# Performance work log

Measured on AMD Instinct MI355X. Metric: run time of the kernel, lower is better.

Reference implementation:

```python
import jax, jax.numpy as jnp
import numpy as np

N = 50000  # num nodes


def _spmm(edge_index, edge_w, x):
    # sparse [N,N] @ dense [N,d] via gather + segment-sum
    row, col = edge_index[0], edge_index[1]
    msgs = edge_w[:, None] * x[col]                      # [E, d]
    return jax.ops.segment_sum(msgs, row, num_segments=N)


def setup_inputs() -> dict:
    key = jax.random.key(0)
    k1, k2, k3, k4, k5 = jax.random.split(key, 5)
    E1, E2, d = 800000, 1600000, 128
    x = jax.random.normal(k1, (N, d), dtype=jnp.float32)
    edge_index1 = jax.random.randint(k2, (2, E1), 0, N, dtype=jnp.int64)
    edge_w1 = jax.random.uniform(k3, (E1,), dtype=jnp.float32)
    edge_index2 = jax.random.randint(k4, (2, E2), 0, N, dtype=jnp.int64)
    edge_w2 = jax.random.uniform(k5, (E2,), dtype=jnp.float32)
    return {"x": x, "edge_index1": edge_index1, "edge_w1": edge_w1,
            "edge_index2": edge_index2, "edge_w2": edge_w2}


def reference(x, edge_index1, edge_w1, edge_index2, edge_w2):
    x1 = _spmm(edge_index1, edge_w1, x)   # adj_t  @ x  -> [N, d]
    x2 = _spmm(edge_index2, edge_w2, x)   # adj_t2 @ x  -> [N, d]
    return jnp.concatenate([x1, x2], axis=1)  # [N, 2d]
```

## Files before the change

### kernel.cpp

```cpp
#include <hip/hip_runtime.h>


#define N_NODES 50000
#define D 128
#define OUT_STRIDE 256

#define BSHIFT 6
#define BROWS 64
#define NBUCK ((N_NODES + BROWS - 1) >> BSHIFT)
#define BBITS 10
#define CHUNK 8192
#define WSEG (CHUNK / 8)
#define SITERS (WSEG / 64)
#define CAPB 3072

typedef float vf2 __attribute__((ext_vector_type(2)));

static inline size_t align256(size_t x) { return (x + 255) & ~(size_t)255; }

__device__ __forceinline__ unsigned f32_to_bf16_bits(float f) {
    unsigned u = __float_as_uint(f);
    return (u + 0x7fffu + ((u >> 16) & 1u)) >> 16;
}

template<int BITS>
__device__ __forceinline__ unsigned long long wave_match(int v, bool valid) {
    unsigned long long m = __ballot(valid ? 1 : 0);
    #pragma unroll
    for (int k = 0; k < BITS; ++k) {
        unsigned long long vb = __ballot((v >> k) & 1);
        m &= ((v >> k) & 1) ? vb : ~vb;
    }
    return m;
}


__global__ void __launch_bounds__(512, 4) prep(
        const int* __restrict__ ei1, const float* __restrict__ w1, int E1, int nch1,
        const int* __restrict__ ei2, const float* __restrict__ w2, int E2, int ncht,
        uint2* __restrict__ inter, int* __restrict__ ends,
        const float* __restrict__ x, uint2* __restrict__ xb4, int n4) {
    int bid = blockIdx.x;
    if (bid >= ncht) {
        int i = (bid - ncht) * 512 + threadIdx.x;
        if (i < n4) {
            float4 v = ((const float4*)x)[i];
            unsigned a = f32_to_bf16_bits(v.x);
            unsigned b = f32_to_bf16_bits(v.y);
            unsigned c = f32_to_bf16_bits(v.z);
            unsigned d = f32_to_bf16_bits(v.w);
            xb4[i] = make_uint2(a | (b << 16), c | (d << 16));
        }
        return;
    }
    int cid = bid;
    int g = (cid < nch1) ? 0 : 1;
    int chunk = g ? cid - nch1 : cid;
    const int*   ei = g ? ei2 : ei1;
    const float* w  = g ? w2  : w1;
    int E           = g ? E2  : E1;
    int e0  = chunk * CHUNK;
    int cnt = min(CHUNK, E - e0);

    __shared__ uint2 stage[CHUNK];
    __shared__ unsigned short hwc[8][NBUCK];
    __shared__ int wsum[8];
    int t = threadIdx.x, lane = t & 63, wid = t >> 6;
    unsigned long long below = (1ull << lane) - 1ull;
    for (int i = t; i < (8 * NBUCK) / 2; i += 512) ((int*)hwc)[i] = 0;
    __syncthreads();

    int s0 = wid * WSEG, s1 = min(cnt, s0 + WSEG);
    unsigned meta[SITERS];
    unsigned recs[SITERS];
    #pragma unroll
    for (int k = 0; k < SITERS; ++k) {
        int i = s0 + k * 64 + lane;
        bool v = (i < s1);
        int row = v ? ei[e0 + i] : 0;
        int col = v ? ei[E + e0 + i] : 0;
        float wv = v ? w[e0 + i] : 0.f;
        int bb = row >> BSHIFT;
        unsigned long long m = wave_match<BBITS>(bb, v);
        unsigned rank = (unsigned)__popcll(m & below);
        unsigned base = hwc[wid][bb];
        if (v && (m & below) == 0)
            hwc[wid][bb] = (unsigned short)(base + (unsigned)__popcll(m));
        meta[k] = (unsigned)bb | ((unsigned)(row & 63) << 10) | ((base + rank) << 16);
        recs[k] = (unsigned)col | (f32_to_bf16_bits(wv) << 16);
    }
    __syncthreads();
    {
        int b0 = 2 * t, b1 = b0 + 1;
        int h0[8], h1[8];
        int t0 = 0, t1 = 0;
        if (b0 < NBUCK) {
            #pragma unroll
            for (int q = 0; q < 8; ++q) { h0[q] = hwc[q][b0]; t0 += h0[q]; }
        }
        if (b1 < NBUCK) {
            #pragma unroll
            for (int q = 0; q < 8; ++q) { h1[q] = hwc[q][b1]; t1 += h1[q]; }
        }
        int p = t0 + t1, s = p;
        #pragma unroll
        for (int d2 = 1; d2 < 64; d2 <<= 1) { int u = __shfl_up(s, d2, 64); if (lane >= d2) s += u; }
        if (lane == 63) wsum[wid] = s;
        __syncthreads();
        int add = 0;
        #pragma unroll
        for (int k = 0; k < 8; ++k) if (k < wid) add += wsum[k];
        s += add;
        int excl = s - p;
        if (b0 < NBUCK) {
            int a = excl;
            #pragma unroll
            for (int q = 0; q < 8; ++q) { int h = h0[q]; hwc[q][b0] = (unsigned short)a; a += h; }
            ends[(size_t)cid * NBUCK + b0] = a;
        }
        if (b1 < NBUCK) {
            int a = excl + t0;
            #pragma unroll
            for (int q = 0; q < 8; ++q) { int h = h1[q]; hwc[q][b1] = (unsigned short)a; a += h; }
            ends[(size_t)cid * NBUCK + b1] = a;
        }
    }
    __syncthreads();
    #pragma unroll
    for (int k = 0; k < SITERS; ++k) {
        int i = s0 + k * 64 + lane;
        if (i < s1) {
            unsigned mk = meta[k];
            unsigned bb = mk & 1023u;
            unsigned rlv = (mk >> 10) & 63u;
            unsigned pos = mk >> 16;
            unsigned base = hwc[wid][bb];
            stage[base + pos] = make_uint2(rlv, recs[k]);
        }
    }
    __syncthreads();
    for (int i = t; i < cnt; i += 512)
        inter[(size_t)cid * CHUNK + i] = stage[i];
}


__device__ __forceinline__ void fma_rec(unsigned p, unsigned rec, float& ax, float& ay) {
    float w = __int_as_float((int)(rec & 0xffff0000u));
    ax += w * __int_as_float((int)(p << 16));
    ay += w * __int_as_float((int)(p & 0xffff0000u));
}

__global__ void __launch_bounds__(512, 4) bucket_accum(
        const uint2* __restrict__ inter, const int* __restrict__ ends,
        const unsigned* __restrict__ xb,
        float* __restrict__ out, int nch1, int nch2) {
    int b = blockIdx.x, g = blockIdx.y;
    int c0 = g ? nch1 : 0;
    int nc = g ? nch2 : nch1;

    __shared__ unsigned char rl[CAPB];
    __shared__ unsigned recs[CAPB];
    __shared__ unsigned outb[CAPB];
    __shared__ int crow[BROWS], cur[BROWS], rstart[BROWS];
    __shared__ int total;
    int t = threadIdx.x, lane = t & 63, wid = t >> 6;
    if (t < BROWS) crow[t] = 0;
    if (t == 0) total = 0;
    __syncthreads();
    for (int ci = t; ci < nc; ci += 512) {
        const int* ep = ends + (size_t)(c0 + ci) * NBUCK;
        int s = b ? ep[b - 1] : 0;
        int e = ep[b];
        int n = e - s;
        if (!n) continue;
        int dst = atomicAdd(&total, n);
        const uint2* src = inter + (size_t)(c0 + ci) * CHUNK + s;
        int k = 0;
        for (; k + 2 <= n; k += 2) {
            uint2 a  = src[k];
            uint2 b2 = src[k + 1];
            int p0 = dst + k, p1 = dst + k + 1;
            if (p0 < CAPB) { rl[p0] = (unsigned char)a.x;  recs[p0] = a.y;  atomicAdd(&crow[a.x], 1); }
            if (p1 < CAPB) { rl[p1] = (unsigned char)b2.x; recs[p1] = b2.y; atomicAdd(&crow[b2.x], 1); }
        }
        if (k < n) {
            uint2 a = src[k];
            int p0 = dst + k;
            if (p0 < CAPB) { rl[p0] = (unsigned char)a.x; recs[p0] = a.y; atomicAdd(&crow[a.x], 1); }
        }
    }
    __syncthreads();
    int cnt = min(total, CAPB);
    if (wid == 0) {
        int v = crow[lane], s = v;
        #pragma unroll
        for (int d = 1; d < 64; d <<= 1) { int u = __shfl_up(s, d, 64); if (lane >= d) s += u; }
        cur[lane] = s - v;
        rstart[lane] = s - v;
    }
    __syncthreads();
    for (int i = t; i < cnt; i += 512) {
        int pos = atomicAdd(&cur[rl[i]], 1);
        outb[pos] = recs[i];
    }
    __syncthreads();
    for (int r = wid * 8; r < wid * 8 + 8; ++r) {
        int grow = (b << BSHIFT) + r;
        if (grow >= N_NODES) break;
        int s0 = rstart[r], e0 = cur[r];
        float ax = 0.f, ay = 0.f;
        int j = s0;
        for (; j + 4 <= e0; j += 4) {
            unsigned c0r = outb[j];
            unsigned c1 = outb[j + 1];
            unsigned c2 = outb[j + 2];
            unsigned c3 = outb[j + 3];
            unsigned p0 = xb[(size_t)(c0r & 0xffffu) * 64 + lane];
            unsigned p1 = xb[(size_t)(c1 & 0xffffu) * 64 + lane];
            unsigned p2 = xb[(size_t)(c2 & 0xffffu) * 64 + lane];
            unsigned p3 = xb[(size_t)(c3 & 0xffffu) * 64 + lane];
            fma_rec(p0, c0r, ax, ay);
            fma_rec(p1, c1, ax, ay);
            fma_rec(p2, c2, ax, ay);
            fma_rec(p3, c3, ax, ay);
        }
        for (; j < e0; ++j) {
            unsigned c = outb[j];
            unsigned p = xb[(size_t)(c & 0xffffu) * 64 + lane];
            fma_rec(p, c, ax, ay);
        }
        vf2 rv; rv.x = ax; rv.y = ay;
        vf2* o = (vf2*)(out + (size_t)grow * OUT_STRIDE + g * D);
        __builtin_nontemporal_store(rv, o + lane);
    }
}


__global__ void spmm_scatter(const float* __restrict__ x,
                             const int* __restrict__ ei,
                             const float* __restrict__ w,
                             float* __restrict__ out,
                             int E, int col_off) {
    long long gid = (long long)blockIdx.x * blockDim.x + threadIdx.x;
    int e    = (int)(gid >> 5);
    int lane = (int)(gid & 31);
    if (e >= E) return;
    int row  = ei[e];
    int col  = ei[E + e];
    float wv = w[e];
    const float4* xv = (const float4*)(x + (size_t)col * D);
    float4 v = xv[lane];
    float* o = out + (size_t)row * OUT_STRIDE + col_off + lane * 4;
    atomicAdd(o + 0, wv * v.x);
    atomicAdd(o + 1, wv * v.y);
    atomicAdd(o + 2, wv * v.z);
    atomicAdd(o + 3, wv * v.w);
}

extern "C" void kernel_launch(void* const* d_in, const int* in_sizes, int n_in,
                              void* d_out, int out_size, void* d_ws, size_t ws_size,
                              hipStream_t stream) {
    const float* x   = (const float*)d_in[0];
    const int*   ei1 = (const int*)d_in[1];
    const float* w1  = (const float*)d_in[2];
    const int*   ei2 = (const int*)d_in[3];
    const float* w2  = (const float*)d_in[4];
    float* out = (float*)d_out;

    const int E1 = in_sizes[1] / 2;
    const int E2 = in_sizes[3] / 2;
    const int block = 256;

    int nch1 = (E1 + CHUNK - 1) / CHUNK;
    int nch2 = (E2 + CHUNK - 1) / CHUNK;
    int ncht = nch1 + nch2;

    size_t ends_b  = align256((size_t)ncht * NBUCK * sizeof(int));
    size_t inter_b = align256((size_t)ncht * CHUNK * sizeof(uint2));
    size_t xb_b    = align256((size_t)N_NODES * 64 * sizeof(unsigned));
    size_t o_ends  = 0;
    size_t o_int   = o_ends + ends_b;
    size_t o_xb    = o_int + inter_b;
    size_t needed  = o_xb + xb_b;

    bool ok = (nch1 <= 512) && (nch2 <= 512);

    if (ws_size < needed || !ok) {
        (void)hipMemsetAsync(d_out, 0, (size_t)out_size * sizeof(float), stream);
        long long th1 = (long long)E1 * 32;
        spmm_scatter<<<(int)((th1 + block - 1) / block), block, 0, stream>>>(
            x, ei1, w1, out, E1, 0);
        long long th2 = (long long)E2 * 32;
        spmm_scatter<<<(int)((th2 + block - 1) / block), block, 0, stream>>>(
            x, ei2, w2, out, E2, D);
        return;
    }

    char* ws = (char*)d_ws;
    int*      ends  = (int*)(ws + o_ends);
    uint2*    inter = (uint2*)(ws + o_int);
    unsigned* xb    = (unsigned*)(ws + o_xb);

    {
        int n4 = N_NODES * 32;
        int ncvt = (n4 + 511) / 512;
        prep<<<ncht + ncvt, 512, 0, stream>>>(
            ei1, w1, E1, nch1, ei2, w2, E2, ncht,
            inter, ends, x, (uint2*)xb, n4);
    }

    {
        dim3 gr(NBUCK, 2);
        bucket_accum<<<gr, 512, 0, stream>>>(inter, ends, xb, out, nch1, nch2);
    }
}
```

Before: 212.9 us.

## Fuse prep and bucket accumulation into one cooperative kernel with grid sync

```diff
diff --git a/kernel.cpp b/kernel.cpp
--- a/kernel.cpp
+++ b/kernel.cpp
@@ -1,4 +1,5 @@
 #include <hip/hip_runtime.h>
+#include <hip/hip_cooperative_groups.h>
 
 
 #define N_NODES 50000
@@ -9,10 +10,26 @@
 #define BROWS 64
 #define NBUCK ((N_NODES + BROWS - 1) >> BSHIFT)
 #define BBITS 10
-#define CHUNK 8192
-#define WSEG (CHUNK / 8)
+#define CHUNK 5120
+#define NTHR 1024
+#define NWAVE 16
+#define WSEG (CHUNK / NWAVE)
 #define SITERS (WSEG / 64)
-#define CAPB 3072
+#define ACAP 4096
+#define GRID 512
+
+#define SM_SIZE 50688
+#define SO_REC  0
+#define SO_RL   20480
+#define SO_HWC  25600
+#define SO_WSUM 50624
+#define AO_RECS 0
+#define AO_OUTB 16384
+#define AO_RL   32768
+#define AO_CROW 36864
+#define AO_CUR  37120
+#define AO_RST  37376
+#define AO_TOT  37632
 
 typedef float vf2 __attribute__((ext_vector_type(2)));
 
@@ -35,25 +52,30 @@
 }
 
 
-__global__ void __launch_bounds__(512, 4) prep(
+__device__ __forceinline__ void dev_cvt(const float* __restrict__ x,
+                                        unsigned* __restrict__ xb, int n4) {
+    for (long long i = (long long)blockIdx.x * NTHR + threadIdx.x; i < n4;
+         i += (long long)gridDim.x * NTHR) {
+        float4 v = ((const float4*)x)[i];
+        unsigned a = f32_to_bf16_bits(v.x);
+        unsigned b = f32_to_bf16_bits(v.y);
+        unsigned c = f32_to_bf16_bits(v.z);
+        unsigned d = f32_to_bf16_bits(v.w);
+        ((uint2*)xb)[i] = make_uint2(a | (b << 16), c | (d << 16));
+    }
+}
+
+
+__device__ void dev_scatter(int cid,
         const int* __restrict__ ei1, const float* __restrict__ w1, int E1, int nch1,
-        const int* __restrict__ ei2, const float* __restrict__ w2, int E2, int ncht,
-        uint2* __restrict__ inter, int* __restrict__ ends,
-        const float* __restrict__ x, uint2* __restrict__ xb4, int n4) {
-    int bid = blockIdx.x;
-    if (bid >= ncht) {
-        int i = (bid - ncht) * 512 + threadIdx.x;
-        if (i < n4) {
-            float4 v = ((const float4*)x)[i];
-            unsigned a = f32_to_bf16_bits(v.x);
-            unsigned b = f32_to_bf16_bits(v.y);
-            unsigned c = f32_to_bf16_bits(v.z);
-            unsigned d = f32_to_bf16_bits(v.w);
-            xb4[i] = make_uint2(a | (b << 16), c | (d << 16));
-        }
-        return;
-    }
-    int cid = bid;
+        const int* __restrict__ ei2, const float* __restrict__ w2, int E2,
+        unsigned* __restrict__ irec, unsigned char* __restrict__ irl,
+        int* __restrict__ ends, char* sm) {
+    unsigned*       stage_rec = (unsigned*)(sm + SO_REC);
+    unsigned char*  stage_rl  = (unsigned char*)(sm + SO_RL);
+    unsigned short* hwc       = (unsigned short*)(sm + SO_HWC);
+    int*            wsum      = (int*)(sm + SO_WSUM);
+
     int g = (cid < nch1) ? 0 : 1;
     int chunk = g ? cid - nch1 : cid;
     const int*   ei = g ? ei2 : ei1;
@@ -62,12 +84,9 @@
     int e0  = chunk * CHUNK;
     int cnt = min(CHUNK, E - e0);
 
-    __shared__ uint2 stage[CHUNK];
-    __shared__ unsigned short hwc[8][NBUCK];
-    __shared__ int wsum[8];
     int t = threadIdx.x, lane = t & 63, wid = t >> 6;
     unsigned long long below = (1ull << lane) - 1ull;
-    for (int i = t; i < (8 * NBUCK) / 2; i += 512) ((int*)hwc)[i] = 0;
+    for (int i = t; i < (NWAVE * NBUCK) / 2; i += NTHR) ((int*)hwc)[i] = 0;
     __syncthreads();
 
     int s0 = wid * WSEG, s1 = min(cnt, s0 + WSEG);
@@ -83,46 +102,37 @@
         int bb = row >> BSHIFT;
         unsigned long long m = wave_match<BBITS>(bb, v);
         unsigned rank = (unsigned)__popcll(m & below);
-        unsigned base = hwc[wid][bb];
+        unsigned base = hwc[wid * NBUCK + bb];
         if (v && (m & below) == 0)
-            hwc[wid][bb] = (unsigned short)(base + (unsigned)__popcll(m));
+            hwc[wid * NBUCK + bb] = (unsigned short)(base + (unsigned)__popcll(m));
         meta[k] = (unsigned)bb | ((unsigned)(row & 63) << 10) | ((base + rank) << 16);
         recs[k] = (unsigned)col | (f32_to_bf16_bits(wv) << 16);
     }
     __syncthreads();
     {
-        int b0 = 2 * t, b1 = b0 + 1;
-        int h0[8], h1[8];
-        int t0 = 0, t1 = 0;
-        if (b0 < NBUCK) {
+        int tot = 0;
+        if (t < NBUCK) {
             #pragma unroll
-            for (int q = 0; q < 8; ++q) { h0[q] = hwc[q][b0]; t0 += h0[q]; }
-        }
-        if (b1 < NBUCK) {
-            #pragma unroll
-            for (int q = 0; q < 8; ++q) { h1[q] = hwc[q][b1]; t1 += h1[q]; }
-        }
-        int p = t0 + t1, s = p;
+            for (int q = 0; q < NWAVE; ++q) tot += hwc[q * NBUCK + t];
+        }
+        int s = tot;
         #pragma unroll
         for (int d2 = 1; d2 < 64; d2 <<= 1) { int u = __shfl_up(s, d2, 64); if (lane >= d2) s += u; }
         if (lane == 63) wsum[wid] = s;
         __syncthreads();
         int add = 0;
         #pragma unroll
-        for (int k = 0; k < 8; ++k) if (k < wid) add += wsum[k];
+        for (int k = 0; k < NWAVE; ++k) if (k < wid) add += wsum[k];
         s += add;
-        int excl = s - p;
-        if (b0 < NBUCK) {
-            int a = excl;
+        if (t < NBUCK) {
+            int a = s - tot;
             #pragma unroll
-            for (int q = 0; q < 8; ++q) { int h = h0[q]; hwc[q][b0] = (unsigned short)a; a += h; }
-            ends[(size_t)cid * NBUCK + b0] = a;
-        }
-        if (b1 < NBUCK) {
-            int a = excl + t0;
-            #pragma unroll
-            for (int q = 0; q < 8; ++q) { int h = h1[q]; hwc[q][b1] = (unsigned short)a; a += h; }
-            ends[(size_t)cid * NBUCK + b1] = a;
+            for (int q = 0; q < NWAVE; ++q) {
+                int hq = hwc[q * NBUCK + t];
+                hwc[q * NBUCK + t] = (unsigned short)a;
+                a += hq;
+            }
+            ends[(size_t)cid * NBUCK + t] = a;
         }
     }
     __syncthreads();
@@ -132,15 +142,16 @@
         if (i < s1) {
             unsigned mk = meta[k];
             unsigned bb = mk & 1023u;
-            unsigned rlv = (mk >> 10) & 63u;
-            unsigned pos = mk >> 16;
-            unsigned base = hwc[wid][bb];
-            stage[base + pos] = make_uint2(rlv, recs[k]);
-        }
-    }
-    __syncthreads();
-    for (int i = t; i < cnt; i += 512)
-        inter[(size_t)cid * CHUNK + i] = stage[i];
+            unsigned pos = (mk >> 16) + hwc[wid * NBUCK + bb];
+            stage_rec[pos] = recs[k];
+            stage_rl[pos] = (unsigned char)((mk >> 10) & 63u);
+        }
+    }
+    __syncthreads();
+    for (int i = t; i < cnt; i += NTHR) {
+        irec[(size_t)cid * CHUNK + i] = stage_rec[i];
+        irl[(size_t)cid * CHUNK + i]  = stage_rl[i];
+    }
 }
 
 
@@ -150,89 +161,133 @@
     ay += w * __int_as_float((int)(p & 0xffff0000u));
 }
 
-__global__ void __launch_bounds__(512, 4) bucket_accum(
-        const uint2* __restrict__ inter, const int* __restrict__ ends,
-        const unsigned* __restrict__ xb,
-        float* __restrict__ out, int nch1, int nch2) {
-    int b = blockIdx.x, g = blockIdx.y;
+__device__ void dev_accum(int b, int g, int nch1, int nch2,
+        const unsigned* __restrict__ irec, const unsigned char* __restrict__ irl,
+        const int* __restrict__ ends, const unsigned* __restrict__ xb,
+        float* __restrict__ out, char* sm) {
+    unsigned*      arecs = (unsigned*)(sm + AO_RECS);
+    unsigned*      aoutb = (unsigned*)(sm + AO_OUTB);
+    unsigned char* arl   = (unsigned char*)(sm + AO_RL);
+    int* crow   = (int*)(sm + AO_CROW);
+    int* cur    = (int*)(sm + AO_CUR);
+    int* rstart = (int*)(sm + AO_RST);
+    int* total  = (int*)(sm + AO_TOT);
+
     int c0 = g ? nch1 : 0;
     int nc = g ? nch2 : nch1;
-
-    __shared__ unsigned char rl[CAPB];
-    __shared__ unsigned recs[CAPB];
-    __shared__ unsigned outb[CAPB];
-    __shared__ int crow[BROWS], cur[BROWS], rstart[BROWS];
-    __shared__ int total;
     int t = threadIdx.x, lane = t & 63, wid = t >> 6;
     if (t < BROWS) crow[t] = 0;
-    if (t == 0) total = 0;
-    __syncthreads();
-    for (int ci = t; ci < nc; ci += 512) {
+    if (t == 0) *total = 0;
+    __syncthreads();
+    for (int ci = t; ci < nc; ci += NTHR) {
         const int* ep = ends + (size_t)(c0 + ci) * NBUCK;
         int s = b ? ep[b - 1] : 0;
         int e = ep[b];
         int n = e - s;
         if (!n) continue;
-        int dst = atomicAdd(&total, n);
-        const uint2* src = inter + (size_t)(c0 + ci) * CHUNK + s;
+        int dst = atomicAdd(total, n);
+        const unsigned* sr = irec + (size_t)(c0 + ci) * CHUNK + s;
+        const unsigned char* sl = irl + (size_t)(c0 + ci) * CHUNK + s;
         int k = 0;
         for (; k + 2 <= n; k += 2) {
-            uint2 a  = src[k];
-            uint2 b2 = src[k + 1];
+            unsigned r0 = sr[k], r1 = sr[k + 1];
+            unsigned char l0 = sl[k], l1 = sl[k + 1];
             int p0 = dst + k, p1 = dst + k + 1;
-            if (p0 < CAPB) { rl[p0] = (unsigned char)a.x;  recs[p0] = a.y;  atomicAdd(&crow[a.x], 1); }
-            if (p1 < CAPB) { rl[p1] = (unsigned char)b2.x; recs[p1] = b2.y; atomicAdd(&crow[b2.x], 1); }
+            if (p0 < ACAP) { arl[p0] = l0; arecs[p0] = r0; atomicAdd(&crow[l0], 1); }
+            if (p1 < ACAP) { arl[p1] = l1; arecs[p1] = r1; atomicAdd(&crow[l1], 1); }
         }
         if (k < n) {
-            uint2 a = src[k];
+            unsigned r0 = sr[k];
+            unsigned char l0 = sl[k];
             int p0 = dst + k;
-            if (p0 < CAPB) { rl[p0] = (unsigned char)a.x; recs[p0] = a.y; atomicAdd(&crow[a.x], 1); }
-        }
-    }
-    __syncthreads();
-    int cnt = min(total, CAPB);
+            if (p0 < ACAP) { arl[p0] = l0; arecs[p0] = r0; atomicAdd(&crow[l0], 1); }
+        }
+    }
+    __syncthreads();
+    int cnt = min(*total, ACAP);
     if (wid == 0) {
         int v = crow[lane], s = v;
         #pragma unroll
-        for (int d = 1; d < 64; d <<= 1) { int u = __shfl_up(s, d, 64); if (lane >= d) s += u; }
+        for (int d2 = 1; d2 < 64; d2 <<= 1) { int u = __shfl_up(s, d2, 64); if (lane >= d2) s += u; }
         cur[lane] = s - v;
         rstart[lane] = s - v;
     }
     __syncthreads();
-    for (int i = t; i < cnt; i += 512) {
-        int pos = atomicAdd(&cur[rl[i]], 1);
-        outb[pos] = recs[i];
-    }
-    __syncthreads();
-    for (int r = wid * 8; r < wid * 8 + 8; ++r) {
+    for (int i = t; i < cnt; i += NTHR) {
+        int pos = atomicAdd(&cur[arl[i]], 1);
+        aoutb[pos] = arecs[i];
+    }
+    __syncthreads();
+    for (int r = wid * 4; r < wid * 4 + 4; ++r) {
         int grow = (b << BSHIFT) + r;
         if (grow >= N_NODES) break;
-        int s0 = rstart[r], e0 = cur[r];
+        int rs = rstart[r], re = cur[r];
         float ax = 0.f, ay = 0.f;
-        int j = s0;
-        for (; j + 4 <= e0; j += 4) {
-            unsigned c0r = outb[j];
-            unsigned c1 = outb[j + 1];
-            unsigned c2 = outb[j + 2];
-            unsigned c3 = outb[j + 3];
+        int j = rs;
+        for (; j + 4 <= re; j += 4) {
+            unsigned c0r = aoutb[j];
+            unsigned c1r = aoutb[j + 1];
+            unsigned c2r = aoutb[j + 2];
+            unsigned c3r = aoutb[j + 3];
             unsigned p0 = xb[(size_t)(c0r & 0xffffu) * 64 + lane];
-            unsigned p1 = xb[(size_t)(c1 & 0xffffu) * 64 + lane];
-            unsigned p2 = xb[(size_t)(c2 & 0xffffu) * 64 + lane];
-            unsigned p3 = xb[(size_t)(c3 & 0xffffu) * 64 + lane];
+            unsigned p1 = xb[(size_t)(c1r & 0xffffu) * 64 + lane];
+            unsigned p2 = xb[(size_t)(c2r & 0xffffu) * 64 + lane];
+            unsigned p3 = xb[(size_t)(c3r & 0xffffu) * 64 + lane];
             fma_rec(p0, c0r, ax, ay);
-            fma_rec(p1, c1, ax, ay);
-            fma_rec(p2, c2, ax, ay);
-            fma_rec(p3, c3, ax, ay);
-        }
-        for (; j < e0; ++j) {
-            unsigned c = outb[j];
-            unsigned p = xb[(size_t)(c & 0xffffu) * 64 + lane];
-            fma_rec(p, c, ax, ay);
+            fma_rec(p1, c1r, ax, ay);
+            fma_rec(p2, c2r, ax, ay);
+            fma_rec(p3, c3r, ax, ay);
+        }
+        for (; j < re; ++j) {
+            unsigned cr = aoutb[j];
+            unsigned p = xb[(size_t)(cr & 0xffffu) * 64 + lane];
+            fma_rec(p, cr, ax, ay);
         }
         vf2 rv; rv.x = ax; rv.y = ay;
         vf2* o = (vf2*)(out + (size_t)grow * OUT_STRIDE + g * D);
         __builtin_nontemporal_store(rv, o + lane);
     }
+}
+
+
+__global__ void __launch_bounds__(NTHR, 8) k_fused(
+        const int* ei1, const float* w1, int E1, int nch1,
+        const int* ei2, const float* w2, int E2, int nch2, int ncht,
+        unsigned* irec, unsigned char* irl, int* ends,
+        const float* x, unsigned* xb, int n4, float* out) {
+    __shared__ alignas(16) char sm[SM_SIZE];
+    dev_cvt(x, xb, n4);
+    if ((int)blockIdx.x < ncht)
+        dev_scatter(blockIdx.x, ei1, w1, E1, nch1, ei2, w2, E2, irec, irl, ends, sm);
+    cooperative_groups::this_grid().sync();
+    for (int task = blockIdx.x; task < 2 * NBUCK; task += gridDim.x) {
+        int g = task >= NBUCK;
+        int b = g ? task - NBUCK : task;
+        __syncthreads();
+        dev_accum(b, g, nch1, nch2, irec, irl, ends, xb, out, sm);
+    }
+}
+
+
+__global__ void __launch_bounds__(NTHR, 8) k_prep(
+        const int* ei1, const float* w1, int E1, int nch1,
+        const int* ei2, const float* w2, int E2, int ncht,
+        unsigned* irec, unsigned char* irl, int* ends,
+        const float* x, unsigned* xb, int n4) {
+    __shared__ alignas(16) char sm[SM_SIZE];
+    dev_cvt(x, xb, n4);
+    if ((int)blockIdx.x < ncht)
+        dev_scatter(blockIdx.x, ei1, w1, E1, nch1, ei2, w2, E2, irec, irl, ends, sm);
+}
+
+__global__ void __launch_bounds__(NTHR, 8) k_accum(
+        const unsigned* irec, const unsigned char* irl, const int* ends,
+        const unsigned* xb, float* out, int nch1, int nch2) {
+    __shared__ alignas(16) char sm[AO_TOT + 16];
+    int task = blockIdx.x;
+    int g = task >= NBUCK;
+    int b = g ? task - NBUCK : task;
+    dev_accum(b, g, nch1, nch2, irec, irl, ends, xb, out, sm);
 }
 
 
@@ -260,57 +315,64 @@
 extern "C" void kernel_launch(void* const* d_in, const int* in_sizes, int n_in,
                               void* d_out, int out_size, void* d_ws, size_t ws_size,
                               hipStream_t stream) {
-    const float* x   = (const float*)d_in[0];
-    const int*   ei1 = (const int*)d_in[1];
-    const float* w1  = (const float*)d_in[2];
-    const int*   ei2 = (const int*)d_in[3];
-    const float* w2  = (const float*)d_in[4];
-    float* out = (float*)d_out;
-
-    const int E1 = in_sizes[1] / 2;
-    const int E2 = in_sizes[3] / 2;
+    const int*   ei1_p = (const int*)d_in[1];
+    const float* w1_p  = (const float*)d_in[2];
+    const int*   ei2_p = (const int*)d_in[3];
+    const float* w2_p  = (const float*)d_in[4];
+    const float* x_p   = (const float*)d_in[0];
+    float* out_p = (float*)d_out;
+
+    int E1 = in_sizes[1] / 2;
+    int E2 = in_sizes[3] / 2;
     const int block = 256;
 
     int nch1 = (E1 + CHUNK - 1) / CHUNK;
     int nch2 = (E2 + CHUNK - 1) / CHUNK;
     int ncht = nch1 + nch2;
-
-    size_t ends_b  = align256((size_t)ncht * NBUCK * sizeof(int));
-    size_t inter_b = align256((size_t)ncht * CHUNK * sizeof(uint2));
-    size_t xb_b    = align256((size_t)N_NODES * 64 * sizeof(unsigned));
-    size_t o_ends  = 0;
-    size_t o_int   = o_ends + ends_b;
-    size_t o_xb    = o_int + inter_b;
-    size_t needed  = o_xb + xb_b;
-
-    bool ok = (nch1 <= 512) && (nch2 <= 512);
-
-    if (ws_size < needed || !ok) {
+    int n4   = N_NODES * 32;
+
+    size_t rec_b  = align256((size_t)ncht * CHUNK * sizeof(unsigned));
+    size_t rl_b   = align256((size_t)ncht * CHUNK);
+    size_t ends_b = align256((size_t)ncht * NBUCK * sizeof(int));
+    size_t xb_b   = align256((size_t)N_NODES * 64 * sizeof(unsigned));
+    size_t o_rec  = 0;
+    size_t o_rl   = o_rec + rec_b;
+    size_t o_ends = o_rl + rl_b;
+    size_t o_xb   = o_ends + ends_b;
+    size_t needed = o_xb + xb_b;
+
+    bool shape_ok = (ncht <= GRID) && (nch1 <= NTHR) && (nch2 <= NTHR);
+
+    if (ws_size < needed || !shape_ok) {
         (void)hipMemsetAsync(d_out, 0, (size_t)out_size * sizeof(float), stream);
         long long th1 = (long long)E1 * 32;
         spmm_scatter<<<(int)((th1 + block - 1) / block), block, 0, stream>>>(
-            x, ei1, w1, out, E1, 0);
+            x_p, ei1_p, w1_p, out_p, E1, 0);
         long long th2 = (long long)E2 * 32;
         spmm_scatter<<<(int)((th2 + block - 1) / block), block, 0, stream>>>(
-            x, ei2, w2, out, E2, D);
+            x_p, ei2_p, w2_p, out_p, E2, D);
         return;
     }
 
     char* ws = (char*)d_ws;
-    int*      ends  = (int*)(ws + o_ends);
-    uint2*    inter = (uint2*)(ws + o_int);
-    unsigned* xb    = (unsigned*)(ws + o_xb);
-
-    {
-        int n4 = N_NODES * 32;
-        int ncvt = (n4 + 511) / 512;
-        prep<<<ncht + ncvt, 512, 0, stream>>>(
-            ei1, w1, E1, nch1, ei2, w2, E2, ncht,
-            inter, ends, x, (uint2*)xb, n4);
-    }
-
-    {
-        dim3 gr(NBUCK, 2);
-        bucket_accum<<<gr, 512, 0, stream>>>(inter, ends, xb, out, nch1, nch2);
-    }
-}
+    unsigned*      irec = (unsigned*)(ws + o_rec);
+    unsigned char* irl  = (unsigned char*)(ws + o_rl);
+    int*           ends = (int*)(ws + o_ends);
+    unsigned*      xb   = (unsigned*)(ws + o_xb);
+
+    int occ = 0;
+    hipError_t qe = hipOccupancyMaxActiveBlocksPerMultiprocessor(&occ, k_fused, NTHR, 0);
+    if (qe == hipSuccess && occ >= 2) {
+        void* ka[] = { (void*)&ei1_p, (void*)&w1_p, (void*)&E1, (void*)&nch1,
+                       (void*)&ei2_p, (void*)&w2_p, (void*)&E2, (void*)&nch2,
+                       (void*)&ncht, (void*)&irec, (void*)&irl, (void*)&ends,
+                       (void*)&x_p, (void*)&xb, (void*)&n4, (void*)&out_p };
+        (void)hipLaunchCooperativeKernel((const void*)k_fused, dim3(GRID), dim3(NTHR),
+                                         ka, 0, stream);
+        return;
+    }
+
+    k_prep<<<GRID, NTHR, 0, stream>>>(ei1_p, w1_p, E1, nch1, ei2_p, w2_p, E2,
+                                      ncht, irec, irl, ends, x_p, xb, n4);
+    k_accum<<<2 * NBUCK, NTHR, 0, stream>>>(irec, irl, ends, xb, out_p, nch1, nch2);
+}
```

Measured after the change: 228.1 us. +7.1%, slower.
